# Kernel tuning notes

Measured on AMD Instinct MI355X. Metric: run time of the kernel, lower is better.

## Reference

```python
import jax, jax.numpy as jnp
import numpy as np

D = 128
N_COLS = 64
EPS = 1e-6
# op MLP index per feature token: mult, add, cos, absdiff, sub_ab, sub_ba, div_ab, div_ba
MLP_IDX = np.array([0, 1, 2, 3, 4, 4, 5, 5])


def setup_inputs() -> dict:
    key = jax.random.key(0)
    ks = jax.random.split(key, 16)
    B = 64
    pairs = np.array([(i, j) for i in range(N_COLS) for j in range(i + 1, N_COLS)], dtype=np.int32)
    P = pairs.shape[0]  # 2016
    s = 0.02
    inp = {
        "x": jax.random.normal(ks[0], (B, N_COLS, D), dtype=jnp.float32),
        "presence": jax.random.randint(ks[1], (B, N_COLS), 0, 2, dtype=jnp.int32),
        "idx_i": jnp.asarray(pairs[:, 0]),
        "idx_j": jnp.asarray(pairs[:, 1]),
        # 6 op MLPs (multiply, add, cosine, abs_diff, subtract, divide): d -> d/2 -> d
        "ops_W1": jax.random.normal(ks[2], (6, D, D // 2), dtype=jnp.float32) * s,
        "ops_b1": jnp.zeros((6, D // 2), dtype=jnp.float32),
        "ops_W2": jax.random.normal(ks[3], (6, D // 2, D), dtype=jnp.float32) * s,
        "ops_b2": jnp.zeros((6, D), dtype=jnp.float32),
        # presence MLP: 4 -> d/2 -> d
        "pres_W1": jax.random.normal(ks[4], (4, D // 2), dtype=jnp.float32) * s,
        "pres_b1": jnp.zeros((D // 2,), dtype=jnp.float32),
        "pres_W2": jax.random.normal(ks[5], (D // 2, D), dtype=jnp.float32) * s,
        "pres_b2": jnp.zeros((D,), dtype=jnp.float32),
        # fusion MLP: 9d -> 2d -> d
        "fus_W1": jax.random.normal(ks[6], (9 * D, 2 * D), dtype=jnp.float32) * s,
        "fus_b1": jnp.zeros((2 * D,), dtype=jnp.float32),
        "fus_W2": jax.random.normal(ks[7], (2 * D, D), dtype=jnp.float32) * s,
        "fus_b2": jnp.zeros((D,), dtype=jnp.float32),
    }
    return inp


def reference(x, presence, idx_i, idx_j,
              ops_W1, ops_b1, ops_W2, ops_b2,
              pres_W1, pres_b1, pres_W2, pres_b2,
              fus_W1, fus_b1, fus_W2, fus_b2):
    B = x.shape[0]
    P = idx_i.shape[0]
    A = x[:, idx_i]  # [B, P, D]
    Bv = x[:, idx_j]  # [B, P, D]
    An = A / (jnp.linalg.norm(A, axis=-1, keepdims=True) + EPS)
    Bn = Bv / (jnp.linalg.norm(Bv, axis=-1, keepdims=True) + EPS)
    # 8 elementwise relation features [8, B, P, D]
    feats = jnp.stack([
        A * Bv,                 # multiply
        A + Bv,                 # add
        An * Bn,                # cosine (elementwise normalized product)
        jnp.abs(A - Bv),        # abs diff
        A - Bv,                 # subtract A->B
        Bv - A,                 # subtract B->A
        A / (Bv + EPS),         # divide A/B
        Bv / (A + EPS),         # divide B/A
    ])
    W1 = ops_W1[MLP_IDX]  # [8, D, D/2]
    b1 = ops_b1[MLP_IDX]
    W2 = ops_W2[MLP_IDX]
    b2 = ops_b2[MLP_IDX]
    h = jax.nn.relu(jnp.einsum('kbpd,kdh->kbph', feats, W1) + b1[:, None, None, :])
    tok = jnp.einsum('kbph,khd->kbpd', h, W2) + b2[:, None, None, :]  # [8, B, P, D]
    # presence flags [B, P, 4]
    pa = presence[:, idx_i].astype(x.dtype)
    pb = presence[:, idx_j].astype(x.dtype)
    flags = jnp.stack([pa * pb, pa * (1 - pb), (1 - pa) * pb, (1 - pa) * (1 - pb)], axis=-1)
    ptok = jax.nn.relu(flags @ pres_W1 + pres_b1) @ pres_W2 + pres_b2  # [B, P, D]
    # concat 9 tokens -> fusion MLP -> 1 token per pair
    cat = jnp.concatenate([jnp.transpose(tok, (1, 2, 0, 3)).reshape(B, P, 8 * D), ptok], axis=-1)
    out = jax.nn.relu(cat @ fus_W1 + fus_b1) @ fus_W2 + fus_b2  # [B, P, D]
    return out
```

## Files before the change

### kernel.cpp

```cpp
#include <hip/hip_runtime.h>

#define EPS 1e-6f

using bfrag = __attribute__((ext_vector_type(8))) short;
using hfrag = __attribute__((ext_vector_type(8))) _Float16;
using ffrag = __attribute__((ext_vector_type(4))) float;
typedef unsigned short ushortT;

#define MFMA(a, b, c) __builtin_amdgcn_mfma_f32_16x16x32_bf16((a), (b), (c), 0, 0, 0)
#define MFMA16(a, b, c) __builtin_amdgcn_mfma_f32_16x16x32_f16((a), (b), (c), 0, 0, 0)

__device__ __forceinline__ ushortT bf_hi(float x) {
  unsigned u = __builtin_bit_cast(unsigned, x);
  return (ushortT)((u + 0x7FFFu + ((u >> 16) & 1u)) >> 16);
}
__device__ __forceinline__ float uaf(unsigned u) { return __builtin_bit_cast(float, u); }
__device__ __forceinline__ unsigned cvtpk(float a, float b) {
  unsigned d;
  asm("v_cvt_pk_bf16_f32 %0, %1, %2" : "=v"(d) : "v"(a), "v"(b));
  return d;
}
__device__ __forceinline__ unsigned pkf16(float a, float b) {
  unsigned d;
  asm("v_cvt_pkrtz_f16_f32 %0, %1, %2" : "=v"(d) : "v"(a), "v"(b));
  return d;
}
__device__ __forceinline__ int op_of(int k) { return (k < 4) ? k : ((k >> 1) + 2); }

__global__ void prologue(const float* __restrict__ ops_W1,
                         const float* __restrict__ ops_W2,
                         const float* __restrict__ ops_b2,
                         const float* __restrict__ pres_W1,
                         const float* __restrict__ pres_b1,
                         const float* __restrict__ pres_W2,
                         const float* __restrict__ pres_b2,
                         const float* __restrict__ fus_W1,
                         const float* __restrict__ fus_b1,
                         const float* __restrict__ fus_W2,
                         ushortT* __restrict__ Gp,
                         ushortT* __restrict__ W1p,
                         ushortT* __restrict__ W2p,
                         float* __restrict__ cb) {
  const int blk = blockIdx.x;
  const int tid = threadIdx.x;

  if (blk < 512) {
    int r = blk, n = tid;
    int slot = r >> 6;
    const int KMAP[8] = {0, 2, 3, 4, 1, 5, 6, 7};
    int k = KMAP[slot];
    int op = op_of(k);
    const float* w2 = ops_W2 + (size_t)(op * 64 + (r & 63)) * 128;
    const float* w1 = fus_W1 + (size_t)(k * 128) * 256 + n;
    float a0 = 0.f, a1 = 0.f, a2 = 0.f, a3 = 0.f;
#pragma unroll 8
    for (int d = 0; d < 128; d += 4) {
      a0 = fmaf(w2[d], w1[(size_t)d * 256], a0);
      a1 = fmaf(w2[d + 1], w1[(size_t)(d + 1) * 256], a1);
      a2 = fmaf(w2[d + 2], w1[(size_t)(d + 2) * 256], a2);
      a3 = fmaf(w2[d + 3], w1[(size_t)(d + 3) * 256], a3);
    }
    float acc = (a0 + a1) + (a2 + a3);
    ushortT outv;
    if (slot < 6) {
      _Float16 hv = (_Float16)acc;
      outv = __builtin_bit_cast(ushortT, hv);
    } else {
      outv = bf_hi(acc);
    }
    int nt = n >> 4, kk = r >> 5, quad = (r >> 3) & 3, j = r & 7;
    int lane = quad * 16 + (n & 15);
    Gp[((nt * 16 + kk) * 64 + lane) * 8 + j] = outv;
  } else if (blk < 544) {
    int gid = (blk - 512) * 256 + tid;
    int lane = gid & 63, kk = (gid >> 6) & 3, nt = (gid >> 8) & 3, k = gid >> 10;
    int op = op_of(k);
    int col = nt * 16 + (lane & 15);
#pragma unroll
    for (int j = 0; j < 8; ++j) {
      int d = kk * 32 + ((lane >> 4) & 3) * 8 + j;
      float w = ops_W1[((size_t)op * 128 + d) * 64 + col];
      ushortT outv;
      if (k < 6) {
        _Float16 hv = (_Float16)w;
        outv = __builtin_bit_cast(ushortT, hv);
      } else {
        outv = bf_hi(w);
      }
      W1p[gid * 8 + j] = outv;
    }
  } else if (blk < 560) {
    int gid = (blk - 544) * 256 + tid;
    int lane = gid & 63, kk = (gid >> 6) & 7, nt = gid >> 9;
    int col = nt * 16 + (lane & 15);
#pragma unroll
    for (int j = 0; j < 8; ++j) {
      int d = kk * 32 + ((lane >> 4) & 3) * 8 + j;
      W2p[gid * 8 + j] = bf_hi(fus_W2[(size_t)d * 128 + col]);
    }
  } else {
    int c = blk - 560, n = tid;
    __shared__ float hrelu[64];
    __shared__ float ptok[128];
    if (n < 64) hrelu[n] = fmaxf(pres_W1[c * 64 + n] + pres_b1[n], 0.f);
    __syncthreads();
    if (n < 128) {
      float p0 = pres_b2[n], p1 = 0.f;
#pragma unroll 8
      for (int hh = 0; hh < 64; hh += 2) {
        p0 = fmaf(hrelu[hh], pres_W2[hh * 128 + n], p0);
        p1 = fmaf(hrelu[hh + 1], pres_W2[(hh + 1) * 128 + n], p1);
      }
      ptok[n] = p0 + p1;
    }
    __syncthreads();
    float acc = fus_b1[n];
#pragma unroll 4
    for (int d = 0; d < 128; ++d)
      acc = fmaf(ptok[d], fus_W1[(size_t)(1024 + d) * 256 + n], acc);
    float acc2 = 0.f;
    for (int k = 0; k < 8; ++k) {
      int op = op_of(k);
#pragma unroll 4
      for (int d = 0; d < 128; ++d)
        acc2 = fmaf(ops_b2[op * 128 + d], fus_W1[(size_t)(k * 128 + d) * 256 + n], acc2);
    }
    cb[c * 256 + n] = acc + acc2;
  }
}

__device__ __forceinline__ void ldX(const float* Xrow, int quad, float (&r)[32]) {
#pragma unroll
  for (int kk = 0; kk < 4; ++kk) {
    float4 t0 = *(const float4*)(Xrow + kk * 32 + quad * 8);
    float4 t1 = *(const float4*)(Xrow + kk * 32 + quad * 8 + 4);
    r[kk * 8 + 0] = t0.x; r[kk * 8 + 1] = t0.y; r[kk * 8 + 2] = t0.z; r[kk * 8 + 3] = t0.w;
    r[kk * 8 + 4] = t1.x; r[kk * 8 + 5] = t1.y; r[kk * 8 + 6] = t1.z; r[kk * 8 + 7] = t1.w;
  }
}

struct Frag2 {
  bfrag h[4];
  bfrag l[4];
};

union U4 {
  unsigned u[4];
  bfrag b;
};

#define FM_MUL 0
#define FM_ADD 1
#define FM_SUB 2
#define FM_ABS 3
#define FM_DAB 4
#define FM_DBA 5

template <int M>
__device__ __forceinline__ void buildFragsF16(const float (&af)[32], const float (&bf)[32],
                                              bfrag (&h)[4]) {
#pragma unroll
  for (int kk = 0; kk < 4; ++kk) {
    U4 uh;
#pragma unroll
    for (int p = 0; p < 4; ++p) {
      float a0 = af[kk * 8 + 2 * p],     b0 = bf[kk * 8 + 2 * p];
      float a1 = af[kk * 8 + 2 * p + 1], b1 = bf[kk * 8 + 2 * p + 1];
      float f0, f1;
      if constexpr (M == FM_MUL)      { f0 = a0 * b0; f1 = a1 * b1; }
      else if constexpr (M == FM_ADD) { f0 = a0 + b0; f1 = a1 + b1; }
      else if constexpr (M == FM_SUB) { f0 = a0 - b0; f1 = a1 - b1; }
      else                            { f0 = fabsf(a0 - b0); f1 = fabsf(a1 - b1); }
      uh.u[p] = pkf16(f0, f1);
    }
    h[kk] = uh.b;
  }
}

template <int M>
__device__ __forceinline__ void buildFrags(const float (&af)[32], const float (&bf)[32],
                                           Frag2& fr) {
#pragma unroll
  for (int kk = 0; kk < 4; ++kk) {
    U4 uh, ul;
#pragma unroll
    for (int p = 0; p < 4; ++p) {
      float a0 = af[kk * 8 + 2 * p],     b0 = bf[kk * 8 + 2 * p];
      float a1 = af[kk * 8 + 2 * p + 1], b1 = bf[kk * 8 + 2 * p + 1];
      float f0, f1;
      if constexpr (M == FM_DAB) {
        f0 = a0 * __builtin_amdgcn_rcpf(b0 + EPS);
        f1 = a1 * __builtin_amdgcn_rcpf(b1 + EPS);
      } else {
        f0 = b0 * __builtin_amdgcn_rcpf(a0 + EPS);
        f1 = b1 * __builtin_amdgcn_rcpf(a1 + EPS);
      }
      unsigned dh = cvtpk(f0, f1);
      float r0 = f0 - uaf(dh << 16);
      float r1 = f1 - uaf(dh & 0xFFFF0000u);
      uh.u[p] = dh;
      ul.u[p] = cvtpk(r0, r1);
    }
    fr.h[kk] = uh.b;
    fr.l[kk] = ul.b;
  }
}

template <int K>
__device__ __forceinline__ void mmAllF16(const bfrag (&h)[4], int lane,
                                         const ushortT* __restrict__ W1p, ffrag (&s)[4]) {
#pragma unroll
  for (int nt = 0; nt < 4; ++nt) {
    const ushortT* wp = W1p + ((K * 4 + nt) * 4) * 512 + lane * 8;
    ffrag acc = {0.f, 0.f, 0.f, 0.f};
#pragma unroll
    for (int kk = 0; kk < 4; ++kk) {
      hfrag w = __builtin_bit_cast(hfrag, *(const bfrag*)(wp + kk * 512));
      acc = MFMA16(__builtin_bit_cast(hfrag, h[kk]), w, acc);
    }
    s[nt] = acc;
  }
}

template <int K>
__device__ __forceinline__ void mmAll(const Frag2& fr, int lane,
                                      const ushortT* __restrict__ W1p, ffrag (&s)[4]) {
#pragma unroll
  for (int nt = 0; nt < 4; ++nt) {
    const ushortT* wp = W1p + ((K * 4 + nt) * 4) * 512 + lane * 8;
    ffrag acc = {0.f, 0.f, 0.f, 0.f};
#pragma unroll
    for (int kk = 0; kk < 4; ++kk) {
      bfrag w = *(const bfrag*)(wp + kk * 512);
      acc = MFMA(fr.h[kk], w, acc);
      acc = MFMA(fr.l[kk], w, acc);
    }
    s[nt] = acc;
  }
}

__device__ __forceinline__ void ldBias(const float* __restrict__ ops_b1, int OP, int c0,
                                       float (&bb)[4]) {
#pragma unroll
  for (int nt = 0; nt < 4; ++nt) bb[nt] = ops_b1[OP * 64 + nt * 16 + c0];
}

__device__ __forceinline__ void storeHf(ffrag s, float scl, float bias, int rbase, int col,
                                        ushortT (*Hh)[136]) {
  float v[4];
#pragma unroll
  for (int i = 0; i < 4; ++i) v[i] = fmaxf(fmaf(s[i], scl, bias), 0.f);
#pragma unroll
  for (int p = 0; p < 2; ++p) {
    unsigned d = pkf16(v[2 * p], v[2 * p + 1]);
    Hh[rbase + 2 * p][col] = (ushortT)(d & 0xFFFFu);
    Hh[rbase + 2 * p + 1][col] = (ushortT)(d >> 16);
  }
}

__device__ __forceinline__ void storeHf4(const ffrag (&s)[4], float scl, const float (&bb)[4],
                                         int rbase, int colbase, int c0,
                                         ushortT (*Hh)[136]) {
#pragma unroll
  for (int nt = 0; nt < 4; ++nt)
    storeHf(s[nt], scl, bb[nt], rbase, colbase + nt * 16 + c0, Hh);
}

__device__ __forceinline__ void storeH(ffrag s, float bias, int rbase, int col,
                                       ushortT (*Hh)[136], ushortT (*Hl)[136]) {
  float v[4];
#pragma unroll
  for (int i = 0; i < 4; ++i) v[i] = fmaxf(s[i] + bias, 0.f);
#pragma unroll
  for (int p = 0; p < 2; ++p) {
    unsigned dh = cvtpk(v[2 * p], v[2 * p + 1]);
    float r0 = v[2 * p] - uaf(dh << 16);
    float r1 = v[2 * p + 1] - uaf(dh & 0xFFFF0000u);
    unsigned dl = cvtpk(r0, r1);
    Hh[rbase + 2 * p][col] = (ushortT)(dh & 0xFFFFu);
    Hh[rbase + 2 * p + 1][col] = (ushortT)(dh >> 16);
    Hl[rbase + 2 * p][col] = (ushortT)(dl & 0xFFFFu);
    Hl[rbase + 2 * p + 1][col] = (ushortT)(dl >> 16);
  }
}

__device__ __forceinline__ void storeH4(const ffrag (&s)[4], const float (&bb)[4],
                                        int rbase, int colbase, int c0,
                                        ushortT (*Hh)[136], ushortT (*Hl)[136]) {
#pragma unroll
  for (int nt = 0; nt < 4; ++nt)
    storeH(s[nt], bb[nt], rbase, colbase + nt * 16 + c0, Hh, Hl);
}

__device__ __forceinline__ void p3roundF16(int r, int wv, int lane, int quad, int c0,
                                           ushortT (*Hh)[136],
                                           const ushortT* __restrict__ Gp,
                                           ffrag (&u)[4], ffrag (&v)[4]) {
#pragma unroll
  for (int kk = 0; kk < 4; ++kk) {
    hfrag ah0 = __builtin_bit_cast(hfrag, *(const bfrag*)&Hh[c0][kk * 32 + quad * 8]);
    hfrag ah1 = __builtin_bit_cast(hfrag, *(const bfrag*)&Hh[16 + c0][kk * 32 + quad * 8]);
#pragma unroll
    for (int nt4 = 0; nt4 < 4; ++nt4) {
      hfrag g = __builtin_bit_cast(
          hfrag, *(const bfrag*)(Gp + (((wv * 4 + nt4) * 16 + r * 4 + kk) * 64 + lane) * 8));
      u[nt4] = MFMA16(ah0, g, u[nt4]);
      v[nt4] = MFMA16(ah1, g, v[nt4]);
    }
  }
}

__device__ __forceinline__ void p3round(int r, int wv, int lane, int quad, int c0,
                                        ushortT (*Hh)[136], ushortT (*Hl)[136],
                                        const ushortT* __restrict__ Gp,
                                        ffrag (&u)[4], ffrag (&v)[4]) {
#pragma unroll
  for (int kk = 0; kk < 4; ++kk) {
    bfrag ah0 = *(const bfrag*)&Hh[c0][kk * 32 + quad * 8];
    bfrag al0 = *(const bfrag*)&Hl[c0][kk * 32 + quad * 8];
    bfrag ah1 = *(const bfrag*)&Hh[16 + c0][kk * 32 + quad * 8];
    bfrag al1 = *(const bfrag*)&Hl[16 + c0][kk * 32 + quad * 8];
#pragma unroll
    for (int nt4 = 0; nt4 < 4; ++nt4) {
      bfrag g = *(const bfrag*)(Gp + (((wv * 4 + nt4) * 16 + r * 4 + kk) * 64 + lane) * 8);
      u[nt4] = MFMA(ah0, g, u[nt4]);
      u[nt4] = MFMA(al0, g, u[nt4]);
      v[nt4] = MFMA(ah1, g, v[nt4]);
      v[nt4] = MFMA(al1, g, v[nt4]);
    }
  }
}

__global__ __launch_bounds__(256, 3)
void drel_main(const float* __restrict__ x, const int* __restrict__ presence,
               const int* __restrict__ idx_i, const int* __restrict__ idx_j,
               const float* __restrict__ ops_b1, const float* __restrict__ fus_b2,
               const ushortT* __restrict__ W1p, const ushortT* __restrict__ Gp,
               const ushortT* __restrict__ W2p, const float* __restrict__ cbias,
               float* __restrict__ out) {
  __shared__ __align__(16) char smem[51328];
  float   (*Xs)[132]  = reinterpret_cast<float(*)[132]>(smem);
  ushortT (*Hh)[136]  = reinterpret_cast<ushortT(*)[136]>(smem + 33792);
  ushortT (*Hl)[136]  = reinterpret_cast<ushortT(*)[136]>(smem + 42496);
  ushortT (*Dh)[264]  = reinterpret_cast<ushortT(*)[264]>(smem + 33792);
  int* sCombo = reinterpret_cast<int*>(smem + 51200);

  const int tid = threadIdx.x;
  const int wv = tid >> 6, lane = tid & 63, quad = lane >> 4, c0 = lane & 15;
  const int wtile = wv & 1;
  const int wrole = wv >> 1;

  const int blk = blockIdx.x;
  const int b = blk / 63;
  const int p0 = (blk % 63) * 32;

  const float* xb = x + (size_t)b * 64 * 128;
#pragma unroll
  for (int it = 0; it < 8; ++it) {
    int i = tid + it * 256;
    int row = i >> 5, c4 = (i & 31) * 4;
    *(float4*)&Xs[row][c4] = *(const float4*)(xb + row * 128 + c4);
  }
  if (tid < 32) {
    int p = p0 + tid;
    int pa = presence[b * 64 + idx_i[p]];
    int pb = presence[b * 64 + idx_j[p]];
    sCombo[tid] = pa ? (pb ? 0 : 1) : (pb ? 2 : 3);
  }

  const int rI = idx_i[p0 + wtile * 16 + c0];
  const int rJ = idx_j[p0 + wtile * 16 + c0];
  const int rbase = wtile * 16 + quad * 4;

  ffrag u[4], v[4];
  __syncthreads();
  {
    int comb0[4], comb1[4];
#pragma unroll
    for (int i = 0; i < 4; ++i) {
      comb0[i] = sCombo[quad * 4 + i];
      comb1[i] = sCombo[16 + quad * 4 + i];
    }
#pragma unroll
    for (int nt4 = 0; nt4 < 4; ++nt4) {
      int col = (wv * 4 + nt4) * 16 + c0;
#pragma unroll
      for (int i = 0; i < 4; ++i) {
        u[nt4][i] = cbias[comb0[i] * 256 + col];
        v[nt4][i] = cbias[comb1[i] * 256 + col];
      }
    }
  }

  float af[32], bf[32];
  bfrag fh[4];
  ffrag s4[4];

  {
    ldX(Xs[rI], quad, af); ldX(Xs[rJ], quad, bf);
    buildFragsF16<FM_MUL>(af, bf, fh);
    ffrag s[4];
    float bb[4];
    if (wrole == 0) {
      ldBias(ops_b1, 0, c0, bb);
      mmAllF16<0>(fh, lane, W1p, s);
      storeHf4(s, 1.f, bb, rbase, 0, c0, Hh);
    } else {
      float sa = 0.f, sb = 0.f;
#pragma unroll
      for (int q = 0; q < 32; ++q) { sa = fmaf(af[q], af[q], sa); sb = fmaf(bf[q], bf[q], sb); }
      sa += __shfl_xor(sa, 16); sb += __shfl_xor(sb, 16);
      sa += __shfl_xor(sa, 32); sb += __shfl_xor(sb, 32);
      float scl = (1.f / (sqrtf(sa) + EPS)) * (1.f / (sqrtf(sb) + EPS));
      ldBias(ops_b1, 2, c0, bb);
      mmAllF16<2>(fh, lane, W1p, s);
      storeHf4(s, scl, bb, rbase, 64, c0, Hh);
    }
  }
  __syncthreads();
  p3roundF16(0, wv, lane, quad, c0, Hh, Gp, u, v);
  __syncthreads();

  {
    ldX(Xs[rI], quad, af); ldX(Xs[rJ], quad, bf);
    float bb[4];
    if (wrole == 0) {
      buildFragsF16<FM_ABS>(af, bf, fh);
      ffrag s[4];
      ldBias(ops_b1, 3, c0, bb);
      mmAllF16<3>(fh, lane, W1p, s);
      storeHf4(s, 1.f, bb, rbase, 0, c0, Hh);
    } else {
      buildFragsF16<FM_SUB>(af, bf, fh);
      ldBias(ops_b1, 4, c0, bb);
      mmAllF16<4>(fh, lane, W1p, s4);
      storeHf4(s4, 1.f, bb, rbase, 64, c0, Hh);
    }
  }
  __syncthreads();
  p3roundF16(1, wv, lane, quad, c0, Hh, Gp, u, v);
  __syncthreads();

  {
    float bb[4];
    if (wrole == 0) {
      ldX(Xs[rI], quad, af); ldX(Xs[rJ], quad, bf);
      buildFragsF16<FM_ADD>(af, bf, fh);
      ffrag s[4];
      ldBias(ops_b1, 1, c0, bb);
      mmAllF16<1>(fh, lane, W1p, s);
      storeHf4(s, 1.f, bb, rbase, 0, c0, Hh);
    } else {
      ldBias(ops_b1, 4, c0, bb);
      storeHf4(s4, -1.f, bb, rbase, 64, c0, Hh);
    }
  }
  __syncthreads();
  p3roundF16(2, wv, lane, quad, c0, Hh, Gp, u, v);
  __syncthreads();

  {
    ldX(Xs[rI], quad, af); ldX(Xs[rJ], quad, bf);
    Frag2 fr;
    ffrag s[4];
    float bb[4];
    ldBias(ops_b1, 5, c0, bb);
    if (wrole == 0) {
      buildFrags<FM_DAB>(af, bf, fr);
      mmAll<6>(fr, lane, W1p, s);
      storeH4(s, bb, rbase, 0, c0, Hh, Hl);
    } else {
      buildFrags<FM_DBA>(af, bf, fr);
      mmAll<7>(fr, lane, W1p, s);
      storeH4(s, bb, rbase, 64, c0, Hh, Hl);
    }
  }
  __syncthreads();
  p3round(3, wv, lane, quad, c0, Hh, Hl, Gp, u, v);
  __syncthreads();

#pragma unroll
  for (int nt4 = 0; nt4 < 4; ++nt4) {
    int col = (wv * 4 + nt4) * 16 + c0;
#pragma unroll
    for (int p = 0; p < 2; ++p) {
      unsigned du = cvtpk(fmaxf(u[nt4][2 * p], 0.f), fmaxf(u[nt4][2 * p + 1], 0.f));
      Dh[quad * 4 + 2 * p][col] = (ushortT)(du & 0xFFFFu);
      Dh[quad * 4 + 2 * p + 1][col] = (ushortT)(du >> 16);
      unsigned dv = cvtpk(fmaxf(v[nt4][2 * p], 0.f), fmaxf(v[nt4][2 * p + 1], 0.f));
      Dh[16 + quad * 4 + 2 * p][col] = (ushortT)(dv & 0xFFFFu);
      Dh[16 + quad * 4 + 2 * p + 1][col] = (ushortT)(dv >> 16);
    }
  }
  __syncthreads();

  ffrag o[2], q[2];
#pragma unroll
  for (int nt2 = 0; nt2 < 2; ++nt2) {
    float bias = fus_b2[(wv * 2 + nt2) * 16 + c0];
    o[nt2] = ffrag{bias, bias, bias, bias};
    q[nt2] = o[nt2];
  }
#pragma unroll
  for (int kk = 0; kk < 8; ++kk) {
    bfrag dh0 = *(const bfrag*)&Dh[c0][kk * 32 + quad * 8];
    bfrag dh1 = *(const bfrag*)&Dh[16 + c0][kk * 32 + quad * 8];
#pragma unroll
    for (int nt2 = 0; nt2 < 2; ++nt2) {
      bfrag w = *(const bfrag*)(W2p + (((wv * 2 + nt2) * 8 + kk) * 64 + lane) * 8);
      o[nt2] = MFMA(dh0, w, o[nt2]);
      q[nt2] = MFMA(dh1, w, q[nt2]);
    }
  }
#pragma unroll
  for (int nt2 = 0; nt2 < 2; ++nt2) {
    int col = (wv * 2 + nt2) * 16 + c0;
#pragma unroll
    for (int i = 0; i < 4; ++i) {
      int row = quad * 4 + i;
      out[(size_t)(b * 2016 + p0 + row) * 128 + col] = o[nt2][i];
      out[(size_t)(b * 2016 + p0 + 16 + row) * 128 + col] = q[nt2][i];
    }
  }
}

extern "C" void kernel_launch(void* const* d_in, const int* in_sizes, int n_in,
                              void* d_out, int out_size, void* d_ws, size_t ws_size,
                              hipStream_t stream) {
  const float* x        = (const float*)d_in[0];
  const int*   presence = (const int*)d_in[1];
  const int*   idx_i    = (const int*)d_in[2];
  const int*   idx_j    = (const int*)d_in[3];
  const float* ops_W1   = (const float*)d_in[4];
  const float* ops_b1   = (const float*)d_in[5];
  const float* ops_W2   = (const float*)d_in[6];
  const float* ops_b2   = (const float*)d_in[7];
  const float* pres_W1  = (const float*)d_in[8];
  const float* pres_b1  = (const float*)d_in[9];
  const float* pres_W2  = (const float*)d_in[10];
  const float* pres_b2  = (const float*)d_in[11];
  const float* fus_W1   = (const float*)d_in[12];
  const float* fus_b1   = (const float*)d_in[13];
  const float* fus_W2   = (const float*)d_in[14];
  const float* fus_b2   = (const float*)d_in[15];

  char* ws = (char*)d_ws;
  ushortT* Gp  = (ushortT*)(ws);
  ushortT* W1p = (ushortT*)(ws + 262144);
  ushortT* W2p = (ushortT*)(ws + 393216);
  float*   CB  = (float*)(ws + 458752);

  prologue<<<564, 256, 0, stream>>>(ops_W1, ops_W2, ops_b2, pres_W1, pres_b1,
                                    pres_W2, pres_b2, fus_W1, fus_b1, fus_W2,
                                    Gp, W1p, W2p, CB);
  drel_main<<<4032, 256, 0, stream>>>(x, presence, idx_i, idx_j, ops_b1, fus_b2,
                                      W1p, Gp, W2p, CB, (float*)d_out);
}
```

Before: 243.8 us.

## Stage all hidden activations at once and drop x shared-memory staging

Each wave now loads its two x rows directly from global memory instead of first staging the batch's 64x128 x tile in shared memory. It then computes all of its first-layer op MLP outputs into one wide H buffer (520 columns) with a single barrier. The per-round second-stage accumulation then becomes two straight K loops over the full concatenated hidden buffer. This removes roughly seven block barriers and the repeated x reloads from LDS. In exchange the H buffer is larger, register pressure may rise, and the x rows are fetched from global memory (likely L2) by each wave.

Result: slower. 267.8 us (+9.9%).

```diff
diff --git a/kernel.cpp b/kernel.cpp
--- a/kernel.cpp
+++ b/kernel.cpp
@@ -129,7 +129,8 @@
   }
 }
 
-__device__ __forceinline__ void ldX(const float* Xrow, int quad, float (&r)[32]) {
+__device__ __forceinline__ void ldXg(const float* __restrict__ Xrow, int quad,
+                                     float (&r)[32]) {
 #pragma unroll
   for (int kk = 0; kk < 4; ++kk) {
     float4 t0 = *(const float4*)(Xrow + kk * 32 + quad * 8);
@@ -245,8 +246,11 @@
   for (int nt = 0; nt < 4; ++nt) bb[nt] = ops_b1[OP * 64 + nt * 16 + c0];
 }
 
+#define HH_LD 520
+#define HL_LD 136
+
 __device__ __forceinline__ void storeHf(ffrag s, float scl, float bias, int rbase, int col,
-                                        ushortT (*Hh)[136]) {
+                                        ushortT (*Hh)[HH_LD]) {
   float v[4];
 #pragma unroll
   for (int i = 0; i < 4; ++i) v[i] = fmaxf(fmaf(s[i], scl, bias), 0.f);
@@ -260,14 +264,14 @@
 
 __device__ __forceinline__ void storeHf4(const ffrag (&s)[4], float scl, const float (&bb)[4],
                                          int rbase, int colbase, int c0,
-                                         ushortT (*Hh)[136]) {
+                                         ushortT (*Hh)[HH_LD]) {
 #pragma unroll
   for (int nt = 0; nt < 4; ++nt)
     storeHf(s[nt], scl, bb[nt], rbase, colbase + nt * 16 + c0, Hh);
 }
 
-__device__ __forceinline__ void storeH(ffrag s, float bias, int rbase, int col,
-                                       ushortT (*Hh)[136], ushortT (*Hl)[136]) {
+__device__ __forceinline__ void storeH(ffrag s, float bias, int rbase, int colH, int colL,
+                                       ushortT (*Hh)[HH_LD], ushortT (*Hl)[HL_LD]) {
   float v[4];
 #pragma unroll
   for (int i = 0; i < 4; ++i) v[i] = fmaxf(s[i] + bias, 0.f);
@@ -277,58 +281,19 @@
     float r0 = v[2 * p] - uaf(dh << 16);
     float r1 = v[2 * p + 1] - uaf(dh & 0xFFFF0000u);
     unsigned dl = cvtpk(r0, r1);
-    Hh[rbase + 2 * p][col] = (ushortT)(dh & 0xFFFFu);
-    Hh[rbase + 2 * p + 1][col] = (ushortT)(dh >> 16);
-    Hl[rbase + 2 * p][col] = (ushortT)(dl & 0xFFFFu);
-    Hl[rbase + 2 * p + 1][col] = (ushortT)(dl >> 16);
+    Hh[rbase + 2 * p][colH] = (ushortT)(dh & 0xFFFFu);
+    Hh[rbase + 2 * p + 1][colH] = (ushortT)(dh >> 16);
+    Hl[rbase + 2 * p][colL] = (ushortT)(dl & 0xFFFFu);
+    Hl[rbase + 2 * p + 1][colL] = (ushortT)(dl >> 16);
   }
 }
 
 __device__ __forceinline__ void storeH4(const ffrag (&s)[4], const float (&bb)[4],
-                                        int rbase, int colbase, int c0,
-                                        ushortT (*Hh)[136], ushortT (*Hl)[136]) {
+                                        int rbase, int colHbase, int colLbase, int c0,
+                                        ushortT (*Hh)[HH_LD], ushortT (*Hl)[HL_LD]) {
 #pragma unroll
   for (int nt = 0; nt < 4; ++nt)
-    storeH(s[nt], bb[nt], rbase, colbase + nt * 16 + c0, Hh, Hl);
-}
-
-__device__ __forceinline__ void p3roundF16(int r, int wv, int lane, int quad, int c0,
-                                           ushortT (*Hh)[136],
-                                           const ushortT* __restrict__ Gp,
-                                           ffrag (&u)[4], ffrag (&v)[4]) {
-#pragma unroll
-  for (int kk = 0; kk < 4; ++kk) {
-    hfrag ah0 = __builtin_bit_cast(hfrag, *(const bfrag*)&Hh[c0][kk * 32 + quad * 8]);
-    hfrag ah1 = __builtin_bit_cast(hfrag, *(const bfrag*)&Hh[16 + c0][kk * 32 + quad * 8]);
-#pragma unroll
-    for (int nt4 = 0; nt4 < 4; ++nt4) {
-      hfrag g = __builtin_bit_cast(
-          hfrag, *(const bfrag*)(Gp + (((wv * 4 + nt4) * 16 + r * 4 + kk) * 64 + lane) * 8));
-      u[nt4] = MFMA16(ah0, g, u[nt4]);
-      v[nt4] = MFMA16(ah1, g, v[nt4]);
-    }
-  }
-}
-
-__device__ __forceinline__ void p3round(int r, int wv, int lane, int quad, int c0,
-                                        ushortT (*Hh)[136], ushortT (*Hl)[136],
-                                        const ushortT* __restrict__ Gp,
-                                        ffrag (&u)[4], ffrag (&v)[4]) {
-#pragma unroll
-  for (int kk = 0; kk < 4; ++kk) {
-    bfrag ah0 = *(const bfrag*)&Hh[c0][kk * 32 + quad * 8];
-    bfrag al0 = *(const bfrag*)&Hl[c0][kk * 32 + quad * 8];
-    bfrag ah1 = *(const bfrag*)&Hh[16 + c0][kk * 32 + quad * 8];
-    bfrag al1 = *(const bfrag*)&Hl[16 + c0][kk * 32 + quad * 8];
-#pragma unroll
-    for (int nt4 = 0; nt4 < 4; ++nt4) {
-      bfrag g = *(const bfrag*)(Gp + (((wv * 4 + nt4) * 16 + r * 4 + kk) * 64 + lane) * 8);
-      u[nt4] = MFMA(ah0, g, u[nt4]);
-      u[nt4] = MFMA(al0, g, u[nt4]);
-      v[nt4] = MFMA(ah1, g, v[nt4]);
-      v[nt4] = MFMA(al1, g, v[nt4]);
-    }
-  }
+    storeH(s[nt], bb[nt], rbase, colHbase + nt * 16 + c0, colLbase + nt * 16 + c0, Hh, Hl);
 }
 
 __global__ __launch_bounds__(256, 3)
@@ -338,12 +303,11 @@
                const ushortT* __restrict__ W1p, const ushortT* __restrict__ Gp,
                const ushortT* __restrict__ W2p, const float* __restrict__ cbias,
                float* __restrict__ out) {
-  __shared__ __align__(16) char smem[51328];
-  float   (*Xs)[132]  = reinterpret_cast<float(*)[132]>(smem);
-  ushortT (*Hh)[136]  = reinterpret_cast<ushortT(*)[136]>(smem + 33792);
-  ushortT (*Hl)[136]  = reinterpret_cast<ushortT(*)[136]>(smem + 42496);
-  ushortT (*Dh)[264]  = reinterpret_cast<ushortT(*)[264]>(smem + 33792);
-  int* sCombo = reinterpret_cast<int*>(smem + 51200);
+  __shared__ __align__(16) char smem[42112];
+  ushortT (*Hh)[HH_LD] = reinterpret_cast<ushortT(*)[HH_LD]>(smem);
+  ushortT (*Hl)[HL_LD] = reinterpret_cast<ushortT(*)[HL_LD]>(smem + 33280);
+  ushortT (*Dh)[264]   = reinterpret_cast<ushortT(*)[264]>(smem);
+  int* sCombo = reinterpret_cast<int*>(smem + 41984);
 
   const int tid = threadIdx.x;
   const int wv = tid >> 6, lane = tid & 63, quad = lane >> 4, c0 = lane & 15;
@@ -354,13 +318,6 @@
   const int b = blk / 63;
   const int p0 = (blk % 63) * 32;
 
-  const float* xb = x + (size_t)b * 64 * 128;
-#pragma unroll
-  for (int it = 0; it < 8; ++it) {
-    int i = tid + it * 256;
-    int row = i >> 5, c4 = (i & 31) * 4;
-    *(float4*)&Xs[row][c4] = *(const float4*)(xb + row * 128 + c4);
-  }
   if (tid < 32) {
     int p = p0 + tid;
     int pa = presence[b * 64 + idx_i[p]];
@@ -372,8 +329,61 @@
   const int rJ = idx_j[p0 + wtile * 16 + c0];
   const int rbase = wtile * 16 + quad * 4;
 
+  const float* xb = x + (size_t)b * 64 * 128;
+  float af[32], bf[32];
+  ldXg(xb + (size_t)rI * 128, quad, af);
+  ldXg(xb + (size_t)rJ * 128, quad, bf);
+
+  if (wrole == 0) {
+    bfrag fh[4];
+    ffrag s[4];
+    float bb[4];
+    buildFragsF16<FM_MUL>(af, bf, fh);
+    ldBias(ops_b1, 0, c0, bb);
+    mmAllF16<0>(fh, lane, W1p, s);
+    storeHf4(s, 1.f, bb, rbase, 0, c0, Hh);
+    buildFragsF16<FM_ABS>(af, bf, fh);
+    ldBias(ops_b1, 3, c0, bb);
+    mmAllF16<3>(fh, lane, W1p, s);
+    storeHf4(s, 1.f, bb, rbase, 128, c0, Hh);
+    buildFragsF16<FM_ADD>(af, bf, fh);
+    ldBias(ops_b1, 1, c0, bb);
+    mmAllF16<1>(fh, lane, W1p, s);
+    storeHf4(s, 1.f, bb, rbase, 256, c0, Hh);
+    Frag2 fr;
+    buildFrags<FM_DAB>(af, bf, fr);
+    ldBias(ops_b1, 5, c0, bb);
+    mmAll<6>(fr, lane, W1p, s);
+    storeH4(s, bb, rbase, 384, 0, c0, Hh, Hl);
+  } else {
+    bfrag fh[4];
+    ffrag s[4], s4[4];
+    float bb[4];
+    float sa = 0.f, sb = 0.f;
+#pragma unroll
+    for (int q = 0; q < 32; ++q) { sa = fmaf(af[q], af[q], sa); sb = fmaf(bf[q], bf[q], sb); }
+    sa += __shfl_xor(sa, 16); sb += __shfl_xor(sb, 16);
+    sa += __shfl_xor(sa, 32); sb += __shfl_xor(sb, 32);
+    float scl = (1.f / (sqrtf(sa) + EPS)) * (1.f / (sqrtf(sb) + EPS));
+    buildFragsF16<FM_MUL>(af, bf, fh);
+    ldBias(ops_b1, 2, c0, bb);
+    mmAllF16<2>(fh, lane, W1p, s);
+    storeHf4(s, scl, bb, rbase, 64, c0, Hh);
+    buildFragsF16<FM_SUB>(af, bf, fh);
+    ldBias(ops_b1, 4, c0, bb);
+    mmAllF16<4>(fh, lane, W1p, s4);
+    storeHf4(s4, 1.f, bb, rbase, 192, c0, Hh);
+    storeHf4(s4, -1.f, bb, rbase, 320, c0, Hh);
+    Frag2 fr;
+    buildFrags<FM_DBA>(af, bf, fr);
+    ldBias(ops_b1, 5, c0, bb);
+    mmAll<7>(fr, lane, W1p, s);
+    storeH4(s, bb, rbase, 448, 64, c0, Hh, Hl);
+  }
+
+  __syncthreads();
+
   ffrag u[4], v[4];
-  __syncthreads();
   {
     int comb0[4], comb1[4];
 #pragma unroll
@@ -392,91 +402,34 @@
     }
   }
 
-  float af[32], bf[32];
-  bfrag fh[4];
-  ffrag s4[4];
-
-  {
-    ldX(Xs[rI], quad, af); ldX(Xs[rJ], quad, bf);
-    buildFragsF16<FM_MUL>(af, bf, fh);
-    ffrag s[4];
-    float bb[4];
-    if (wrole == 0) {
-      ldBias(ops_b1, 0, c0, bb);
-      mmAllF16<0>(fh, lane, W1p, s);
-      storeHf4(s, 1.f, bb, rbase, 0, c0, Hh);
-    } else {
-      float sa = 0.f, sb = 0.f;
-#pragma unroll
-      for (int q = 0; q < 32; ++q) { sa = fmaf(af[q], af[q], sa); sb = fmaf(bf[q], bf[q], sb); }
-      sa += __shfl_xor(sa, 16); sb += __shfl_xor(sb, 16);
-      sa += __shfl_xor(sa, 32); sb += __shfl_xor(sb, 32);
-      float scl = (1.f / (sqrtf(sa) + EPS)) * (1.f / (sqrtf(sb) + EPS));
-      ldBias(ops_b1, 2, c0, bb);
-      mmAllF16<2>(fh, lane, W1p, s);
-      storeHf4(s, scl, bb, rbase, 64, c0, Hh);
-    }
-  }
-  __syncthreads();
-  p3roundF16(0, wv, lane, quad, c0, Hh, Gp, u, v);
-  __syncthreads();
-
-  {
-    ldX(Xs[rI], quad, af); ldX(Xs[rJ], quad, bf);
-    float bb[4];
-    if (wrole == 0) {
-      buildFragsF16<FM_ABS>(af, bf, fh);
-      ffrag s[4];
-      ldBias(ops_b1, 3, c0, bb);
-      mmAllF16<3>(fh, lane, W1p, s);
-      storeHf4(s, 1.f, bb, rbase, 0, c0, Hh);
-    } else {
-      buildFragsF16<FM_SUB>(af, bf, fh);
-      ldBias(ops_b1, 4, c0, bb);
-      mmAllF16<4>(fh, lane, W1p, s4);
-      storeHf4(s4, 1.f, bb, rbase, 64, c0, Hh);
-    }
-  }
-  __syncthreads();
-  p3roundF16(1, wv, lane, quad, c0, Hh, Gp, u, v);
-  __syncthreads();
-
-  {
-    float bb[4];
-    if (wrole == 0) {
-      ldX(Xs[rI], quad, af); ldX(Xs[rJ], quad, bf);
-      buildFragsF16<FM_ADD>(af, bf, fh);
-      ffrag s[4];
-      ldBias(ops_b1, 1, c0, bb);
-      mmAllF16<1>(fh, lane, W1p, s);
-      storeHf4(s, 1.f, bb, rbase, 0, c0, Hh);
-    } else {
-      ldBias(ops_b1, 4, c0, bb);
-      storeHf4(s4, -1.f, bb, rbase, 64, c0, Hh);
-    }
-  }
-  __syncthreads();
-  p3roundF16(2, wv, lane, quad, c0, Hh, Gp, u, v);
-  __syncthreads();
-
-  {
-    ldX(Xs[rI], quad, af); ldX(Xs[rJ], quad, bf);
-    Frag2 fr;
-    ffrag s[4];
-    float bb[4];
-    ldBias(ops_b1, 5, c0, bb);
-    if (wrole == 0) {
-      buildFrags<FM_DAB>(af, bf, fr);
-      mmAll<6>(fr, lane, W1p, s);
-      storeH4(s, bb, rbase, 0, c0, Hh, Hl);
-    } else {
-      buildFrags<FM_DBA>(af, bf, fr);
-      mmAll<7>(fr, lane, W1p, s);
-      storeH4(s, bb, rbase, 64, c0, Hh, Hl);
-    }
-  }
-  __syncthreads();
-  p3round(3, wv, lane, quad, c0, Hh, Hl, Gp, u, v);
+#pragma unroll
+  for (int KK = 0; KK < 12; ++KK) {
+    hfrag ah0 = __builtin_bit_cast(hfrag, *(const bfrag*)&Hh[c0][KK * 32 + quad * 8]);
+    hfrag ah1 = __builtin_bit_cast(hfrag, *(const bfrag*)&Hh[16 + c0][KK * 32 + quad * 8]);
+#pragma unroll
+    for (int nt4 = 0; nt4 < 4; ++nt4) {
+      hfrag g = __builtin_bit_cast(
+          hfrag, *(const bfrag*)(Gp + (((wv * 4 + nt4) * 16 + KK) * 64 + lane) * 8));
+      u[nt4] = MFMA16(ah0, g, u[nt4]);
+      v[nt4] = MFMA16(ah1, g, v[nt4]);
+    }
+  }
+#pragma unroll
+  for (int KK = 12; KK < 16; ++KK) {
+    bfrag h0 = *(const bfrag*)&Hh[c0][KK * 32 + quad * 8];
+    bfrag l0 = *(const bfrag*)&Hl[c0][(KK - 12) * 32 + quad * 8];
+    bfrag h1 = *(const bfrag*)&Hh[16 + c0][KK * 32 + quad * 8];
+    bfrag l1 = *(const bfrag*)&Hl[16 + c0][(KK - 12) * 32 + quad * 8];
+#pragma unroll
+    for (int nt4 = 0; nt4 < 4; ++nt4) {
+      bfrag g = *(const bfrag*)(Gp + (((wv * 4 + nt4) * 16 + KK) * 64 + lane) * 8);
+      u[nt4] = MFMA(h0, g, u[nt4]);
+      u[nt4] = MFMA(l0, g, u[nt4]);
+      v[nt4] = MFMA(h1, g, v[nt4]);
+      v[nt4] = MFMA(l1, g, v[nt4]);
+    }
+  }
+
   __syncthreads();
 
 #pragma unroll
```

## Stage only referenced X rows in LDS and alias buffers to raise occupancy

Applied to the files above, without the earlier changes.

Each block now computes a bitmask of the rows its 32 pairs actually use, compacts them, and loads only those (at most 40) rows into shared memory instead of all 64. Shared memory shrinks from about 51 KB to about 30 KB by overlaying Hl/Dh on the X staging area, with an extra barrier before Hl is written. Per-thread 32-float register arrays are replaced by on-the-fly LDS reads inside the fragment builders, and launch bounds go from 3 to 4 blocks per SIMD. The intent is higher occupancy and less global traffic, at the cost of repeated LDS reads, atomics and extra syncs.

New measurement: 253.2 us. 3.9% more time.

```diff
diff --git a/kernel.cpp b/kernel.cpp
--- a/kernel.cpp
+++ b/kernel.cpp
@@ -129,15 +129,7 @@
   }
 }
 
-__device__ __forceinline__ void ldX(const float* Xrow, int quad, float (&r)[32]) {
-#pragma unroll
-  for (int kk = 0; kk < 4; ++kk) {
-    float4 t0 = *(const float4*)(Xrow + kk * 32 + quad * 8);
-    float4 t1 = *(const float4*)(Xrow + kk * 32 + quad * 8 + 4);
-    r[kk * 8 + 0] = t0.x; r[kk * 8 + 1] = t0.y; r[kk * 8 + 2] = t0.z; r[kk * 8 + 3] = t0.w;
-    r[kk * 8 + 4] = t1.x; r[kk * 8 + 5] = t1.y; r[kk * 8 + 6] = t1.z; r[kk * 8 + 7] = t1.w;
-  }
-}
+#define XS_ROWS 40
 
 struct Frag2 {
   bfrag h[4];
@@ -157,20 +149,24 @@
 #define FM_DBA 5
 
 template <int M>
-__device__ __forceinline__ void buildFragsF16(const float (&af)[32], const float (&bf)[32],
-                                              bfrag (&h)[4]) {
+__device__ __forceinline__ void buildFragsF16S(const float* RA, const float* RB, int quad,
+                                               bfrag (&h)[4]) {
 #pragma unroll
   for (int kk = 0; kk < 4; ++kk) {
+    float4 a0 = *(const float4*)(RA + kk * 32 + quad * 8);
+    float4 a1 = *(const float4*)(RA + kk * 32 + quad * 8 + 4);
+    float4 b0 = *(const float4*)(RB + kk * 32 + quad * 8);
+    float4 b1 = *(const float4*)(RB + kk * 32 + quad * 8 + 4);
+    float a[8] = {a0.x, a0.y, a0.z, a0.w, a1.x, a1.y, a1.z, a1.w};
+    float b[8] = {b0.x, b0.y, b0.z, b0.w, b1.x, b1.y, b1.z, b1.w};
     U4 uh;
 #pragma unroll
     for (int p = 0; p < 4; ++p) {
-      float a0 = af[kk * 8 + 2 * p],     b0 = bf[kk * 8 + 2 * p];
-      float a1 = af[kk * 8 + 2 * p + 1], b1 = bf[kk * 8 + 2 * p + 1];
       float f0, f1;
-      if constexpr (M == FM_MUL)      { f0 = a0 * b0; f1 = a1 * b1; }
-      else if constexpr (M == FM_ADD) { f0 = a0 + b0; f1 = a1 + b1; }
-      else if constexpr (M == FM_SUB) { f0 = a0 - b0; f1 = a1 - b1; }
-      else                            { f0 = fabsf(a0 - b0); f1 = fabsf(a1 - b1); }
+      if constexpr (M == FM_MUL)      { f0 = a[2*p] * b[2*p]; f1 = a[2*p+1] * b[2*p+1]; }
+      else if constexpr (M == FM_ADD) { f0 = a[2*p] + b[2*p]; f1 = a[2*p+1] + b[2*p+1]; }
+      else if constexpr (M == FM_SUB) { f0 = a[2*p] - b[2*p]; f1 = a[2*p+1] - b[2*p+1]; }
+      else                            { f0 = fabsf(a[2*p] - b[2*p]); f1 = fabsf(a[2*p+1] - b[2*p+1]); }
       uh.u[p] = pkf16(f0, f1);
     }
     h[kk] = uh.b;
@@ -178,22 +174,26 @@
 }
 
 template <int M>
-__device__ __forceinline__ void buildFrags(const float (&af)[32], const float (&bf)[32],
-                                           Frag2& fr) {
+__device__ __forceinline__ void buildFragsS(const float* RA, const float* RB, int quad,
+                                            Frag2& fr) {
 #pragma unroll
   for (int kk = 0; kk < 4; ++kk) {
+    float4 a0 = *(const float4*)(RA + kk * 32 + quad * 8);
+    float4 a1 = *(const float4*)(RA + kk * 32 + quad * 8 + 4);
+    float4 b0 = *(const float4*)(RB + kk * 32 + quad * 8);
+    float4 b1 = *(const float4*)(RB + kk * 32 + quad * 8 + 4);
+    float a[8] = {a0.x, a0.y, a0.z, a0.w, a1.x, a1.y, a1.z, a1.w};
+    float b[8] = {b0.x, b0.y, b0.z, b0.w, b1.x, b1.y, b1.z, b1.w};
     U4 uh, ul;
 #pragma unroll
     for (int p = 0; p < 4; ++p) {
-      float a0 = af[kk * 8 + 2 * p],     b0 = bf[kk * 8 + 2 * p];
-      float a1 = af[kk * 8 + 2 * p + 1], b1 = bf[kk * 8 + 2 * p + 1];
       float f0, f1;
       if constexpr (M == FM_DAB) {
-        f0 = a0 * __builtin_amdgcn_rcpf(b0 + EPS);
-        f1 = a1 * __builtin_amdgcn_rcpf(b1 + EPS);
+        f0 = a[2*p] * __builtin_amdgcn_rcpf(b[2*p] + EPS);
+        f1 = a[2*p+1] * __builtin_amdgcn_rcpf(b[2*p+1] + EPS);
       } else {
-        f0 = b0 * __builtin_amdgcn_rcpf(a0 + EPS);
-        f1 = b1 * __builtin_amdgcn_rcpf(a1 + EPS);
+        f0 = b[2*p] * __builtin_amdgcn_rcpf(a[2*p] + EPS);
+        f1 = b[2*p+1] * __builtin_amdgcn_rcpf(a[2*p+1] + EPS);
       }
       unsigned dh = cvtpk(f0, f1);
       float r0 = f0 - uaf(dh << 16);
@@ -203,6 +203,26 @@
     }
     fr.h[kk] = uh.b;
     fr.l[kk] = ul.b;
+  }
+}
+
+__device__ __forceinline__ void normPass(const float* RA, const float* RB, int quad,
+                                         float& sa, float& sb) {
+  sa = 0.f; sb = 0.f;
+#pragma unroll
+  for (int kk = 0; kk < 4; ++kk) {
+    float4 a0 = *(const float4*)(RA + kk * 32 + quad * 8);
+    float4 a1 = *(const float4*)(RA + kk * 32 + quad * 8 + 4);
+    float4 b0 = *(const float4*)(RB + kk * 32 + quad * 8);
+    float4 b1 = *(const float4*)(RB + kk * 32 + quad * 8 + 4);
+    sa = fmaf(a0.x, a0.x, sa); sa = fmaf(a0.y, a0.y, sa);
+    sa = fmaf(a0.z, a0.z, sa); sa = fmaf(a0.w, a0.w, sa);
+    sa = fmaf(a1.x, a1.x, sa); sa = fmaf(a1.y, a1.y, sa);
+    sa = fmaf(a1.z, a1.z, sa); sa = fmaf(a1.w, a1.w, sa);
+    sb = fmaf(b0.x, b0.x, sb); sb = fmaf(b0.y, b0.y, sb);
+    sb = fmaf(b0.z, b0.z, sb); sb = fmaf(b0.w, b0.w, sb);
+    sb = fmaf(b1.x, b1.x, sb); sb = fmaf(b1.y, b1.y, sb);
+    sb = fmaf(b1.z, b1.z, sb); sb = fmaf(b1.w, b1.w, sb);
   }
 }
 
@@ -331,19 +351,22 @@
   }
 }
 
-__global__ __launch_bounds__(256, 3)
+__global__ __launch_bounds__(256, 4)
 void drel_main(const float* __restrict__ x, const int* __restrict__ presence,
                const int* __restrict__ idx_i, const int* __restrict__ idx_j,
                const float* __restrict__ ops_b1, const float* __restrict__ fus_b2,
                const ushortT* __restrict__ W1p, const ushortT* __restrict__ Gp,
                const ushortT* __restrict__ W2p, const float* __restrict__ cbias,
                float* __restrict__ out) {
-  __shared__ __align__(16) char smem[51328];
+  __shared__ __align__(16) char smem[30464];
   float   (*Xs)[132]  = reinterpret_cast<float(*)[132]>(smem);
-  ushortT (*Hh)[136]  = reinterpret_cast<ushortT(*)[136]>(smem + 33792);
-  ushortT (*Hl)[136]  = reinterpret_cast<ushortT(*)[136]>(smem + 42496);
-  ushortT (*Dh)[264]  = reinterpret_cast<ushortT(*)[264]>(smem + 33792);
-  int* sCombo = reinterpret_cast<int*>(smem + 51200);
+  ushortT (*Hl)[136]  = reinterpret_cast<ushortT(*)[136]>(smem);
+  ushortT (*Dh)[264]  = reinterpret_cast<ushortT(*)[264]>(smem);
+  ushortT (*Hh)[136]  = reinterpret_cast<ushortT(*)[136]>(smem + 21120);
+  int* sCombo = reinterpret_cast<int*>(smem + 29824);
+  unsigned* maskW = reinterpret_cast<unsigned*>(smem + 29952);
+  int* rowLocal = reinterpret_cast<int*>(smem + 29960);
+  int* rowOf = reinterpret_cast<int*>(smem + 30216);
 
   const int tid = threadIdx.x;
   const int wv = tid >> 6, lane = tid & 63, quad = lane >> 4, c0 = lane & 15;
@@ -354,26 +377,39 @@
   const int b = blk / 63;
   const int p0 = (blk % 63) * 32;
 
-  const float* xb = x + (size_t)b * 64 * 128;
-#pragma unroll
-  for (int it = 0; it < 8; ++it) {
-    int i = tid + it * 256;
-    int row = i >> 5, c4 = (i & 31) * 4;
-    *(float4*)&Xs[row][c4] = *(const float4*)(xb + row * 128 + c4);
-  }
+  if (tid < 2) maskW[tid] = 0;
+  __syncthreads();
   if (tid < 32) {
     int p = p0 + tid;
-    int pa = presence[b * 64 + idx_i[p]];
-    int pb = presence[b * 64 + idx_j[p]];
+    int ri = idx_i[p], rj = idx_j[p];
+    int pa = presence[b * 64 + ri];
+    int pb = presence[b * 64 + rj];
     sCombo[tid] = pa ? (pb ? 0 : 1) : (pb ? 2 : 3);
-  }
-
-  const int rI = idx_i[p0 + wtile * 16 + c0];
-  const int rJ = idx_j[p0 + wtile * 16 + c0];
+    atomicOr(&maskW[ri >> 5], 1u << (ri & 31));
+    atomicOr(&maskW[rj >> 5], 1u << (rj & 31));
+  }
+  __syncthreads();
+  const unsigned long long mask =
+      ((unsigned long long)maskW[1] << 32) | (unsigned long long)maskW[0];
+  const int nrows = __popcll(mask);
+  if (tid < 64 && ((mask >> tid) & 1)) {
+    int slot = __popcll(mask & ((1ull << tid) - 1ull));
+    rowLocal[tid] = slot;
+    rowOf[slot] = tid;
+  }
+  __syncthreads();
+
+  const float* xb = x + (size_t)b * 64 * 128;
+  for (int s = tid; s < nrows * 32; s += 256) {
+    int row = s >> 5, c4 = (s & 31) * 4;
+    *(float4*)&Xs[row][c4] = *(const float4*)(xb + (size_t)rowOf[row] * 128 + c4);
+  }
+
+  const int rI = rowLocal[idx_i[p0 + wtile * 16 + c0]];
+  const int rJ = rowLocal[idx_j[p0 + wtile * 16 + c0]];
   const int rbase = wtile * 16 + quad * 4;
 
   ffrag u[4], v[4];
-  __syncthreads();
   {
     int comb0[4], comb1[4];
 #pragma unroll
@@ -391,14 +427,15 @@
       }
     }
   }
-
-  float af[32], bf[32];
+  __syncthreads();
+
+  const float* RA = Xs[rI];
+  const float* RB = Xs[rJ];
   bfrag fh[4];
   ffrag s4[4];
 
   {
-    ldX(Xs[rI], quad, af); ldX(Xs[rJ], quad, bf);
-    buildFragsF16<FM_MUL>(af, bf, fh);
+    buildFragsF16S<FM_MUL>(RA, RB, quad, fh);
     ffrag s[4];
     float bb[4];
     if (wrole == 0) {
@@ -406,9 +443,8 @@
       mmAllF16<0>(fh, lane, W1p, s);
       storeHf4(s, 1.f, bb, rbase, 0, c0, Hh);
     } else {
-      float sa = 0.f, sb = 0.f;
-#pragma unroll
-      for (int q = 0; q < 32; ++q) { sa = fmaf(af[q], af[q], sa); sb = fmaf(bf[q], bf[q], sb); }
+      float sa, sb;
+      normPass(RA, RB, quad, sa, sb);
       sa += __shfl_xor(sa, 16); sb += __shfl_xor(sb, 16);
       sa += __shfl_xor(sa, 32); sb += __shfl_xor(sb, 32);
       float scl = (1.f / (sqrtf(sa) + EPS)) * (1.f / (sqrtf(sb) + EPS));
@@ -422,16 +458,15 @@
   __syncthreads();
 
   {
-    ldX(Xs[rI], quad, af); ldX(Xs[rJ], quad, bf);
     float bb[4];
     if (wrole == 0) {
-      buildFragsF16<FM_ABS>(af, bf, fh);
+      buildFragsF16S<FM_ABS>(RA, RB, quad, fh);
       ffrag s[4];
       ldBias(ops_b1, 3, c0, bb);
       mmAllF16<3>(fh, lane, W1p, s);
       storeHf4(s, 1.f, bb, rbase, 0, c0, Hh);
     } else {
-      buildFragsF16<FM_SUB>(af, bf, fh);
+      buildFragsF16S<FM_SUB>(RA, RB, quad, fh);
       ldBias(ops_b1, 4, c0, bb);
       mmAllF16<4>(fh, lane, W1p, s4);
       storeHf4(s4, 1.f, bb, rbase, 64, c0, Hh);
@@ -444,8 +479,7 @@
   {
     float bb[4];
     if (wrole == 0) {
-      ldX(Xs[rI], quad, af); ldX(Xs[rJ], quad, bf);
-      buildFragsF16<FM_ADD>(af, bf, fh);
+      buildFragsF16S<FM_ADD>(RA, RB, quad, fh);
       ffrag s[4];
       ldBias(ops_b1, 1, c0, bb);
       mmAllF16<1>(fh, lane, W1p, s);
@@ -460,17 +494,17 @@
   __syncthreads();
 
   {
-    ldX(Xs[rI], quad, af); ldX(Xs[rJ], quad, bf);
     Frag2 fr;
+    if (wrole == 0) buildFragsS<FM_DAB>(RA, RB, quad, fr);
+    else            buildFragsS<FM_DBA>(RA, RB, quad, fr);
+    __syncthreads();
     ffrag s[4];
     float bb[4];
     ldBias(ops_b1, 5, c0, bb);
     if (wrole == 0) {
-      buildFrags<FM_DAB>(af, bf, fr);
       mmAll<6>(fr, lane, W1p, s);
       storeH4(s, bb, rbase, 0, c0, Hh, Hl);
     } else {
-      buildFrags<FM_DBA>(af, bf, fr);
       mmAll<7>(fr, lane, W1p, s);
       storeH4(s, bb, rbase, 64, c0, Hh, Hl);
     }
```
